# Kernel tuning notes

Hardware: AMD Instinct MI355X
Metric: run time of the kernel (lower is better)

## Reference

```python
import jax, jax.numpy as jnp
import numpy as np
from itertools import product

# Fixed [27,3] periodic image offsets, matching nn.Parameter(requires_grad=False)
OFFSETS = jnp.asarray(list(product((-1, 0, 1), repeat=3)), dtype=jnp.float32)


def setup_inputs() -> dict:
    B, A = 16384, 64            # structures, atoms per structure
    N = B * A                   # total atoms = 1,048,576
    key = jax.random.key(0)
    k1, k2, k3 = jax.random.split(key, 3)
    # invertible-ish lattice matrices ~ diag(4 Angstrom) + noise
    cell = jnp.eye(3, dtype=jnp.float32)[None] * 4.0 + 0.1 * jax.random.normal(k1, (B, 3, 3), dtype=jnp.float32)
    # fractional coordinates in [0,1)
    x = jax.random.uniform(k2, (N, 3), dtype=jnp.float32)
    x_tilde = x + 0.05 * jax.random.normal(k3, (N, 3), dtype=jnp.float32)
    num_atoms = jnp.full((B,), A, dtype=jnp.int32)
    return {"cell": cell, "x": x, "x_tilde": x_tilde, "num_atoms": num_atoms}


def reference(cell, x, x_tilde, num_atoms):
    B = cell.shape[0]
    N = x.shape[0]
    # batch = arange(B).repeat_interleave(num_atoms), jit-safe via searchsorted
    bounds = jnp.cumsum(num_atoms)
    batch = jnp.searchsorted(bounds, jnp.arange(N), side="right")  # [N]
    cell_b = cell[batch]  # [N,3,3] gather of per-structure cells
    # euc_x_tilde[n,i] = sum_j cell[n,i,j] * x_tilde[n,j]
    euc_xt = jnp.einsum("nij,nj->ni", cell_b, x_tilde)            # [N,3]
    frac = x[:, None, :] + OFFSETS[None, :, :]                    # [N,27,3]
    # euc_x[n,o,i] = sum_j cell[n,i,j] * frac[n,o,j]
    euc_x = jnp.einsum("nij,noj->noi", cell_b, frac)              # [N,27,3]
    dist = jnp.linalg.norm(euc_xt[:, None, :] - euc_x, axis=2)    # [N,27]
    min_idx = jnp.argmin(dist, axis=1)                            # [N]
    shifted = x + OFFSETS[min_idx]                                # [N,3]
    # center = scatter_mean(shifted - x_tilde, batch, dim_size=B)
    sums = jax.ops.segment_sum(shifted - x_tilde, batch, num_segments=B)  # [B,3]
    center = sums / num_atoms.astype(x.dtype)[:, None]
    pred = shifted - center[batch]
    return jnp.mean(jnp.abs(x_tilde - pred))
```

## Files before the change

kernel.cpp:

```cpp
#include <hip/hip_runtime.h>

#define WAVE 64
#define WPB 4
#define SPB (2 * WPB)
#define BLOCK (WAVE * WPB)

__device__ __forceinline__ void argmin_s(const float c[9], float cc2,
                                         float x0, float x1, float x2,
                                         float t0, float t1, float t2,
                                         float& s0, float& s1, float& s2) {
  const float e0 = c[0] * t0 + c[1] * t1 + c[2] * t2;
  const float e1 = c[3] * t0 + c[4] * t1 + c[5] * t2;
  const float e2 = c[6] * t0 + c[7] * t1 + c[8] * t2;
  const float b0 = c[0] * x0 + c[1] * x1 + c[2] * x2;
  const float b1 = c[3] * x0 + c[4] * x1 + c[5] * x2;
  const float b2 = c[6] * x0 + c[7] * x1 + c[8] * x2;
  const float r0 = e0 - b0, r1 = e1 - b1, r2 = e2 - b2;

  unsigned best = 0xFFFFFFFFu;
#pragma unroll
  for (int i = 0; i < 3; ++i) {
    const float di = (float)(i - 1);
    const float p0 = r0 - di * c[0], p1 = r1 - di * c[3], p2 = r2 - di * c[6];
#pragma unroll
    for (int j = 0; j < 3; ++j) {
      const float dj = (float)(j - 1);
      const float q0 = p0 - dj * c[1], q1 = p1 - dj * c[4], q2 = p2 - dj * c[7];
      const float qq = q0 * q0 + q1 * q1 + q2 * q2;
      const float qc = q0 * c[2] + q1 * c[5] + q2 * c[8];
      const float tmp = qq + cc2;
      const float dm = fmaxf(tmp + 2.0f * qc, 0.0f);
      const float dp = fmaxf(tmp - 2.0f * qc, 0.0f);
      const unsigned ob = (unsigned)(9 * i + 3 * j);
      const unsigned km = (__float_as_uint(dm) & ~31u) | (ob + 0u);
      const unsigned k0 = (__float_as_uint(qq) & ~31u) | (ob + 1u);
      const unsigned kp = (__float_as_uint(dp) & ~31u) | (ob + 2u);
      best = min(best, min(km, min(k0, kp)));
    }
  }
  const int o = (int)(best & 31u);
  s0 = x0 + (float)(o / 9 - 1) - t0;
  s1 = x1 + (float)((o / 3) % 3 - 1) - t1;
  s2 = x2 + (float)(o % 3 - 1) - t2;
}

__device__ __forceinline__ float wave_sum(float v) {
#pragma unroll
  for (int m = 32; m >= 1; m >>= 1) v += __shfl_xor(v, m);
  return v;
}

__device__ __forceinline__ int wave_sum_i(int v) {
#pragma unroll
  for (int m = 32; m >= 1; m >>= 1) v += __shfl_xor(v, m);
  return v;
}

__device__ __forceinline__ float structure_fast(const float c[9], float cc2,
                                                bool have, int count,
                                                float x0, float x1, float x2,
                                                float t0, float t1, float t2) {
  float s0 = 0.f, s1 = 0.f, s2 = 0.f;
  if (have) argmin_s(c, cc2, x0, x1, x2, t0, t1, t2, s0, s1, s2);
  const float sx = wave_sum(s0), sy = wave_sum(s1), sz = wave_sum(s2);
  const float inv = 1.0f / (float)count;
  const float cx = sx * inv, cy = sy * inv, cz = sz * inv;
  return have ? (fabsf(cx - s0) + fabsf(cy - s1) + fabsf(cz - s2)) : 0.f;
}

__device__ __forceinline__ float structure_general(const float c[9], float cc2,
                                                   const float* __restrict__ x,
                                                   const float* __restrict__ xt,
                                                   int start, int count, int tid) {
  float sumx = 0.f, sumy = 0.f, sumz = 0.f;
  for (int n = start + tid; n < start + count; n += WAVE) {
    float a0, a1, a2;
    argmin_s(c, cc2, x[3 * n], x[3 * n + 1], x[3 * n + 2],
             xt[3 * n], xt[3 * n + 1], xt[3 * n + 2], a0, a1, a2);
    sumx += a0; sumy += a1; sumz += a2;
  }
  sumx = wave_sum(sumx); sumy = wave_sum(sumy); sumz = wave_sum(sumz);
  const float inv = 1.0f / (float)count;
  const float cx = sumx * inv, cy = sumy * inv, cz = sumz * inv;
  float part = 0.f;
  for (int n = start + tid; n < start + count; n += WAVE) {
    float a0, a1, a2;
    argmin_s(c, cc2, x[3 * n], x[3 * n + 1], x[3 * n + 2],
             xt[3 * n], xt[3 * n + 1], xt[3 * n + 2], a0, a1, a2);
    part += fabsf(cx - a0) + fabsf(cy - a1) + fabsf(cz - a2);
  }
  return part;
}

__global__ __launch_bounds__(BLOCK) void mdl_main(const float* __restrict__ cell,
                                                  const float* __restrict__ x,
                                                  const float* __restrict__ xt,
                                                  const int* __restrict__ na,
                                                  float* __restrict__ partial, int B) {
  __shared__ int ired[WPB];
  __shared__ float wpart[WPB];
  const int wid = __builtin_amdgcn_readfirstlane(threadIdx.x / WAVE);
  const int tid = threadIdx.x % WAVE;
  const int blk8 = blockIdx.x * SPB;

  int s = 0;
  const int nv = blk8 >> 2;
  const int4* na4 = (const int4*)na;
  for (int v = threadIdx.x; v < nv; v += BLOCK) {
    const int4 q = na4[v];
    s += q.x + q.y + q.z + q.w;
  }
  s = wave_sum_i(s);
  if (tid == 0) ired[wid] = s;

  int nloc = 0;
  if (tid < SPB && blk8 + tid < B) nloc = na[blk8 + tid];
  int inc = nloc;
#pragma unroll
  for (int m = 1; m < SPB; m <<= 1) {
    const int u = __shfl_up(inc, m);
    if (tid >= m) inc += u;
  }
  __syncthreads();
  const int base = ired[0] + ired[1] + ired[2] + ired[3];

  const int laneA = 2 * wid, laneB = laneA + 1;
  const int nA = __shfl(nloc, laneA), incA = __shfl(inc, laneA);
  const int nB = __shfl(nloc, laneB), incB = __shfl(inc, laneB);
  const int startA = __builtin_amdgcn_readfirstlane(base + incA - nA);
  const int countA = __builtin_amdgcn_readfirstlane(nA);
  const int startB = __builtin_amdgcn_readfirstlane(base + incB - nB);
  const int countB = __builtin_amdgcn_readfirstlane(nB);
  const int bA = blk8 + laneA;
  const int bB = blk8 + laneB;
  const bool hasA = bA < B;
  const bool hasB = bB < B;

  float part = 0.f;
  if (hasA) {
    float cA[9];
#pragma unroll
    for (int i = 0; i < 9; ++i) cA[i] = cell[9 * bA + i];
    const float ccA = cA[2] * cA[2] + cA[5] * cA[5] + cA[8] * cA[8];
    float cB[9] = {0, 0, 0, 0, 0, 0, 0, 0, 0};
    float ccB = 0.f;
    if (hasB) {
#pragma unroll
      for (int i = 0; i < 9; ++i) cB[i] = cell[9 * bB + i];
      ccB = cB[2] * cB[2] + cB[5] * cB[5] + cB[8] * cB[8];
    }

    if (countA <= WAVE && (!hasB || countB <= WAVE)) {
      const bool haveA = tid < countA;
      const bool haveB = hasB && tid < countB;
      float xA0 = 0, xA1 = 0, xA2 = 0, tA0 = 0, tA1 = 0, tA2 = 0;
      float xB0 = 0, xB1 = 0, xB2 = 0, tB0 = 0, tB1 = 0, tB2 = 0;
      if (haveA) {
        const int n = startA + tid;
        xA0 = x[3 * n]; xA1 = x[3 * n + 1]; xA2 = x[3 * n + 2];
        tA0 = xt[3 * n]; tA1 = xt[3 * n + 1]; tA2 = xt[3 * n + 2];
      }
      if (haveB) {
        const int n = startB + tid;
        xB0 = x[3 * n]; xB1 = x[3 * n + 1]; xB2 = x[3 * n + 2];
        tB0 = xt[3 * n]; tB1 = xt[3 * n + 1]; tB2 = xt[3 * n + 2];
      }
      part += structure_fast(cA, ccA, haveA, countA, xA0, xA1, xA2, tA0, tA1, tA2);
      if (hasB)
        part += structure_fast(cB, ccB, haveB, countB, xB0, xB1, xB2, tB0, tB1, tB2);
    } else {
      part += structure_general(cA, ccA, x, xt, startA, countA, tid);
      if (hasB) part += structure_general(cB, ccB, x, xt, startB, countB, tid);
    }
  }

  part = wave_sum(part);
  if (tid == 0) wpart[wid] = part;
  __syncthreads();
  if (threadIdx.x == 0)
    partial[blockIdx.x] = wpart[0] + wpart[1] + wpart[2] + wpart[3];
}

__global__ __launch_bounds__(256) void mdl_final(const float* __restrict__ partial,
                                                 int nparts, float* __restrict__ out,
                                                 int N) {
  __shared__ double wsum[4];
  double s = 0.0;
  for (int i = threadIdx.x; i < nparts; i += 256) s += (double)partial[i];
#pragma unroll
  for (int m = 32; m >= 1; m >>= 1) s += __shfl_xor(s, m);
  if ((threadIdx.x & (WAVE - 1)) == 0) wsum[threadIdx.x / WAVE] = s;
  __syncthreads();
  if (threadIdx.x == 0) {
    double t = 0.0;
#pragma unroll
    for (int w = 0; w < 4; ++w) t += wsum[w];
    out[0] = (float)(t / (3.0 * (double)N));
  }
}

extern "C" void kernel_launch(void* const* d_in, const int* in_sizes, int n_in,
                              void* d_out, int out_size, void* d_ws, size_t ws_size,
                              hipStream_t stream) {
  const float* cell = (const float*)d_in[0];
  const float* x    = (const float*)d_in[1];
  const float* xt   = (const float*)d_in[2];
  const int*   na   = (const int*)d_in[3];
  const int B = in_sizes[3];
  const int N = in_sizes[1] / 3;

  const int nblocks = (B + SPB - 1) / SPB;
  float* partial = (float*)d_ws;

  mdl_main<<<nblocks, BLOCK, 0, stream>>>(cell, x, xt, na, partial, B);
  mdl_final<<<1, 256, 0, stream>>>(partial, nblocks, (float*)d_out, N);
}
```

Before: 17.98 us.

## Speculatively prefetch atom coordinates assuming uniform atom counts before prefix sum

The kernel guesses each structure's start offset as index times num_atoms[0] and issues the coordinate and cell loads before the num_atoms prefix sum runs. After the scan it checks the guess against the real start and count, and falls back to the general strided path for any structure where it does not match. The aim is to hide the dependency between the prefix sum and the data loads. Block size also doubles to 8 waves, which doubles the structures handled per block and halves the block count, while the prefix loop over num_atoms for earlier blocks stays the same length. The speculative loads cost bandwidth that is wasted when counts vary, but the result stays correct.

```diff
diff --git a/kernel.cpp b/kernel.cpp
--- a/kernel.cpp
+++ b/kernel.cpp
@@ -1,7 +1,7 @@
 #include <hip/hip_runtime.h>
 
 #define WAVE 64
-#define WPB 4
+#define WPB 8
 #define SPB (2 * WPB)
 #define BLOCK (WAVE * WPB)
 
@@ -96,15 +96,50 @@
                                                   const float* __restrict__ x,
                                                   const float* __restrict__ xt,
                                                   const int* __restrict__ na,
-                                                  float* __restrict__ partial, int B) {
+                                                  float* __restrict__ partial,
+                                                  int B, int N) {
   __shared__ int ired[WPB];
   __shared__ float wpart[WPB];
   const int wid = __builtin_amdgcn_readfirstlane(threadIdx.x / WAVE);
   const int tid = threadIdx.x % WAVE;
-  const int blk8 = blockIdx.x * SPB;
+  const int blk = blockIdx.x * SPB;
+
+  const int bA = blk + 2 * wid;
+  const int bB = bA + 1;
+  const bool hasA = bA < B;
+  const bool hasB = bB < B;
+
+  const int na0 = __builtin_amdgcn_readfirstlane(na[0]);
+  const bool spec = (na0 > 0) && (na0 <= WAVE) &&
+                    ((long)(blk + SPB) * (long)na0 <= (long)N);
+
+  float xA0 = 0, xA1 = 0, xA2 = 0, tA0 = 0, tA1 = 0, tA2 = 0;
+  float xB0 = 0, xB1 = 0, xB2 = 0, tB0 = 0, tB1 = 0, tB2 = 0;
+  const int pstartA = bA * na0;
+  const int pstartB = bB * na0;
+  if (spec && hasA && tid < na0) {
+    const int n = pstartA + tid;
+    xA0 = x[3 * n]; xA1 = x[3 * n + 1]; xA2 = x[3 * n + 2];
+    tA0 = xt[3 * n]; tA1 = xt[3 * n + 1]; tA2 = xt[3 * n + 2];
+  }
+  if (spec && hasB && tid < na0) {
+    const int n = pstartB + tid;
+    xB0 = x[3 * n]; xB1 = x[3 * n + 1]; xB2 = x[3 * n + 2];
+    tB0 = xt[3 * n]; tB1 = xt[3 * n + 1]; tB2 = xt[3 * n + 2];
+  }
+  float cA[9] = {0, 0, 0, 0, 0, 0, 0, 0, 0};
+  float cB[9] = {0, 0, 0, 0, 0, 0, 0, 0, 0};
+  if (hasA) {
+#pragma unroll
+    for (int i = 0; i < 9; ++i) cA[i] = cell[9 * bA + i];
+  }
+  if (hasB) {
+#pragma unroll
+    for (int i = 0; i < 9; ++i) cB[i] = cell[9 * bB + i];
+  }
 
   int s = 0;
-  const int nv = blk8 >> 2;
+  const int nv = blk >> 2;
   const int4* na4 = (const int4*)na;
   for (int v = threadIdx.x; v < nv; v += BLOCK) {
     const int4 q = na4[v];
@@ -114,7 +149,7 @@
   if (tid == 0) ired[wid] = s;
 
   int nloc = 0;
-  if (tid < SPB && blk8 + tid < B) nloc = na[blk8 + tid];
+  if (tid < SPB && blk + tid < B) nloc = na[blk + tid];
   int inc = nloc;
 #pragma unroll
   for (int m = 1; m < SPB; m <<= 1) {
@@ -122,7 +157,9 @@
     if (tid >= m) inc += u;
   }
   __syncthreads();
-  const int base = ired[0] + ired[1] + ired[2] + ired[3];
+  int base = 0;
+#pragma unroll
+  for (int w = 0; w < WPB; ++w) base += ired[w];
 
   const int laneA = 2 * wid, laneB = laneA + 1;
   const int nA = __shfl(nloc, laneA), incA = __shfl(inc, laneA);
@@ -131,54 +168,36 @@
   const int countA = __builtin_amdgcn_readfirstlane(nA);
   const int startB = __builtin_amdgcn_readfirstlane(base + incB - nB);
   const int countB = __builtin_amdgcn_readfirstlane(nB);
-  const int bA = blk8 + laneA;
-  const int bB = blk8 + laneB;
-  const bool hasA = bA < B;
-  const bool hasB = bB < B;
+
+  const bool okA = spec && hasA && (startA == pstartA) && (countA == na0);
+  const bool okB = spec && hasB && (startB == pstartB) && (countB == na0);
+
+  const float ccA = cA[2] * cA[2] + cA[5] * cA[5] + cA[8] * cA[8];
+  const float ccB = cB[2] * cB[2] + cB[5] * cB[5] + cB[8] * cB[8];
 
   float part = 0.f;
-  if (hasA) {
-    float cA[9];
-#pragma unroll
-    for (int i = 0; i < 9; ++i) cA[i] = cell[9 * bA + i];
-    const float ccA = cA[2] * cA[2] + cA[5] * cA[5] + cA[8] * cA[8];
-    float cB[9] = {0, 0, 0, 0, 0, 0, 0, 0, 0};
-    float ccB = 0.f;
-    if (hasB) {
-#pragma unroll
-      for (int i = 0; i < 9; ++i) cB[i] = cell[9 * bB + i];
-      ccB = cB[2] * cB[2] + cB[5] * cB[5] + cB[8] * cB[8];
-    }
-
-    if (countA <= WAVE && (!hasB || countB <= WAVE)) {
-      const bool haveA = tid < countA;
-      const bool haveB = hasB && tid < countB;
-      float xA0 = 0, xA1 = 0, xA2 = 0, tA0 = 0, tA1 = 0, tA2 = 0;
-      float xB0 = 0, xB1 = 0, xB2 = 0, tB0 = 0, tB1 = 0, tB2 = 0;
-      if (haveA) {
-        const int n = startA + tid;
-        xA0 = x[3 * n]; xA1 = x[3 * n + 1]; xA2 = x[3 * n + 2];
-        tA0 = xt[3 * n]; tA1 = xt[3 * n + 1]; tA2 = xt[3 * n + 2];
-      }
-      if (haveB) {
-        const int n = startB + tid;
-        xB0 = x[3 * n]; xB1 = x[3 * n + 1]; xB2 = x[3 * n + 2];
-        tB0 = xt[3 * n]; tB1 = xt[3 * n + 1]; tB2 = xt[3 * n + 2];
-      }
-      part += structure_fast(cA, ccA, haveA, countA, xA0, xA1, xA2, tA0, tA1, tA2);
-      if (hasB)
-        part += structure_fast(cB, ccB, haveB, countB, xB0, xB1, xB2, tB0, tB1, tB2);
-    } else {
-      part += structure_general(cA, ccA, x, xt, startA, countA, tid);
-      if (hasB) part += structure_general(cB, ccB, x, xt, startB, countB, tid);
-    }
+  if (okA) {
+    part += structure_fast(cA, ccA, tid < countA, countA,
+                           xA0, xA1, xA2, tA0, tA1, tA2);
+  } else if (hasA && countA > 0) {
+    part += structure_general(cA, ccA, x, xt, startA, countA, tid);
+  }
+  if (okB) {
+    part += structure_fast(cB, ccB, tid < countB, countB,
+                           xB0, xB1, xB2, tB0, tB1, tB2);
+  } else if (hasB && countB > 0) {
+    part += structure_general(cB, ccB, x, xt, startB, countB, tid);
   }
 
   part = wave_sum(part);
   if (tid == 0) wpart[wid] = part;
   __syncthreads();
-  if (threadIdx.x == 0)
-    partial[blockIdx.x] = wpart[0] + wpart[1] + wpart[2] + wpart[3];
+  if (threadIdx.x == 0) {
+    float t = 0.f;
+#pragma unroll
+    for (int w = 0; w < WPB; ++w) t += wpart[w];
+    partial[blockIdx.x] = t;
+  }
 }
 
 __global__ __launch_bounds__(256) void mdl_final(const float* __restrict__ partial,
@@ -212,6 +231,6 @@
   const int nblocks = (B + SPB - 1) / SPB;
   float* partial = (float*)d_ws;
 
-  mdl_main<<<nblocks, BLOCK, 0, stream>>>(cell, x, xt, na, partial, B);
+  mdl_main<<<nblocks, BLOCK, 0, stream>>>(cell, x, xt, na, partial, B, N);
   mdl_final<<<1, 256, 0, stream>>>(partial, nblocks, (float*)d_out, N);
 }
```

Result: no change. 17.84 us (-0.8%).
